# Kernel optimization log

Hardware: AMD Instinct MI355X
Metric: run time of the kernel (lower is better)

Reference implementation:

```python
import jax, jax.numpy as jnp
import numpy as np

N, D_IN, D_HID, D_BOX = 4096, 512, 256, 22
W_SCALE = 0.02  # keep exp(WA) numerically tame


def setup_inputs() -> dict:
    key = jax.random.key(0)
    ks = jax.random.split(key, 10)
    inp = {
        'input_x': jax.random.normal(ks[0], (N, D_IN), dtype=jnp.float32),
        'box': jax.random.normal(ks[1], (N, D_BOX), dtype=jnp.float32),
        # Linear weights stored as [in, out] so y = x @ W
        'WG1': jax.random.normal(ks[2], (D_BOX, D_HID), dtype=jnp.float32) * W_SCALE,
        'WK1': jax.random.normal(ks[3], (D_IN, D_HID), dtype=jnp.float32) * W_SCALE,
        'WQ1': jax.random.normal(ks[4], (D_IN, D_HID), dtype=jnp.float32) * W_SCALE,
        'WV1': jax.random.normal(ks[5], (D_IN, D_HID), dtype=jnp.float32) * W_SCALE,
        'WG2': jax.random.normal(ks[6], (D_BOX, D_HID), dtype=jnp.float32) * W_SCALE,
        'WK2': jax.random.normal(ks[7], (D_IN, D_HID), dtype=jnp.float32) * W_SCALE,
        'WQ2': jax.random.normal(ks[8], (D_IN, D_HID), dtype=jnp.float32) * W_SCALE,
        'WV2': jax.random.normal(ks[9], (D_IN, D_HID), dtype=jnp.float32) * W_SCALE,
    }
    return inp


def _branch(x, box, WG, WK, WQ, WV):
    K = x @ WK                      # [N, 256]
    Q = x @ WQ                      # [N, 256]
    WA = (K @ Q.T) / 16.0           # [N, N]
    G = box @ WG                    # [N, 256]
    WGm = jax.nn.relu((G @ G.T) / 16.0)  # [N, N]
    S = WGm * jnp.exp(WA)           # relu-gated exponential scores
    W = S / jnp.sum(S)              # GLOBAL (whole-matrix) normalization
    return W @ (x @ WV)             # [N, 256]


def reference(input_x, box, WG1, WK1, WQ1, WV1, WG2, WK2, WQ2, WV2):
    FR1 = _branch(input_x, box, WG1, WK1, WQ1, WV1)
    FR2 = _branch(input_x, box, WG2, WK2, WQ2, WV2)
    FR = jnp.concatenate((FR1, FR2), axis=1)  # [N, 512]
    return FR * 0.1 + input_x
```

## Files before the change

### kernel.cpp

```cpp
#include <hip/hip_runtime.h>
#include <hip/hip_bf16.h>
#include <hip/hip_fp16.h>

using bf16 = __hip_bfloat16;
typedef __attribute__((ext_vector_type(8))) short short8;
typedef __attribute__((ext_vector_type(4))) float f32x4;

#define NROW 4096
#define DIN  512
#define DH   256
#define DBOX 22
#define BKU  64
#define KSPL 4

#define NORM_LO 118
#define NORM_HI 130
#define WT_LO   110
#define WT_HI   126

static __device__ __forceinline__ f32x4 mfma16(short8 a, short8 b, f32x4 c) {
  return __builtin_amdgcn_mfma_f32_16x16x32_bf16(a, b, c, 0, 0, 0);
}
static __device__ __forceinline__ short8 ldg8(const bf16* p) {
  return *reinterpret_cast<const short8*>(p);
}
static __device__ __forceinline__ void gll16(const bf16* g, void* lds) {
  __builtin_amdgcn_global_load_lds(
      (const __attribute__((address_space(1))) void*)g,
      (__attribute__((address_space(3))) void*)lds, 16, 0, 0);
}

static __device__ int detect_mode(const void* src, int lo, int hi) {
  __shared__ int cLo, cHi;
  if (threadIdx.x == 0) { cLo = 0; cHi = 0; }
  __syncthreads();
  const unsigned* w = (const unsigned*)src;
  int l = 0, h = 0;
  for (int t = threadIdx.x; t < 1024; t += 256) {
    unsigned v = w[t];
    int elo = (int)((v >> 7) & 0xFF);
    int ehi = (int)((v >> 23) & 0xFF);
    l += (elo >= lo && elo <= hi) ? 1 : 0;
    h += (ehi >= lo && ehi <= hi) ? 1 : 0;
  }
#pragma unroll
  for (int off = 32; off > 0; off >>= 1) {
    l += __shfl_down(l, off, 64);
    h += __shfl_down(h, off, 64);
  }
  if ((threadIdx.x & 63) == 0) { atomicAdd(&cLo, l); atomicAdd(&cHi, h); }
  __syncthreads();
  int lowCnt = cLo, hiCnt = cHi;
  __syncthreads();
  if (lowCnt > 700) return 1;
  if (hiCnt  > 700) return 0;
  return 2;
}

static __device__ __forceinline__ float load_as_float(const void* src, long i, int mode) {
  if (mode == 1) return __bfloat162float(((const bf16*)src)[i]);
  if (mode == 0) return ((const float*)src)[i];
  return __half2float(((const __half*)src)[i]);
}

static __device__ __forceinline__ void store_as(void* dst, long i, float v, int mode) {
  if (mode == 1)      ((bf16*)dst)[i]   = __float2bfloat16(v);
  else if (mode == 2) ((__half*)dst)[i] = __float2half(v);
  else                ((float*)dst)[i]  = v;
}

struct PrepArgs {
  const void* src[4]; bf16* dst[4];
  const void* wsrc[6]; bf16* wdst[6];
};

__global__ __launch_bounds__(256) void prep_kernel(PrepArgs a) {
  __shared__ float tile[64][65];
  if (blockIdx.x < 8588) {
    int b = blockIdx.x, seg, base;
    if (b < 8192)      { seg = 0; base = b; }
    else if (b < 8544) { seg = 1; base = b - 8192; }
    else if (b < 8566) { seg = 2; base = b - 8544; }
    else               { seg = 3; base = b - 8566; }
    int lo = (seg < 2) ? NORM_LO : WT_LO;
    int hi = (seg < 2) ? NORM_HI : WT_HI;
    int mode = detect_mode(a.src[seg], lo, hi);
    int i = base * 256 + threadIdx.x;
    a.dst[seg][i] = __float2bfloat16(load_as_float(a.src[seg], i, mode));
  } else {
    int b2 = blockIdx.x - 8588;
    const int which = b2 >> 5;
    int rem = b2 & 31;
    const int tr = (rem & 7) * 64;
    const int tc = (rem >> 3) * 64;
    int mode = detect_mode(a.wsrc[which], WT_LO, WT_HI);
    const int rin = threadIdx.x >> 6;
    const int cin = threadIdx.x & 63;
#pragma unroll
    for (int p = 0; p < 16; ++p) {
      int r = rin + p * 4;
      tile[r][cin] = load_as_float(a.wsrc[which], (long)(tr + r) * DH + tc + cin, mode);
    }
    __syncthreads();
#pragma unroll
    for (int p = 0; p < 16; ++p) {
      int r = rin + p * 4;
      a.wdst[which][(long)(tc + r) * DIN + tr + cin] = __float2bfloat16(tile[cin][r]);
    }
  }
}

struct ProjArgs { const bf16* Wcat[2]; bf16* CK[2]; bf16* CQ[2]; bf16* VT[2]; };

__global__ __launch_bounds__(256, 3) void proj_kernel(const bf16* __restrict__ X, ProjArgs a) {
  const int z = blockIdx.z;
  const bf16* __restrict__ W = a.Wcat[z];
  __shared__ __align__(16) bf16 Xa[128 * BKU], Wb[128 * BKU];
  const int tid = threadIdx.x;
  const int wave = tid >> 6, lane = tid & 63;
  const int quad = lane >> 4, l16 = lane & 15;
  const int i0 = blockIdx.x * 128, n0 = blockIdx.y * 128;
  const int rw = (wave & 1) * 64, cw = (wave >> 1) * 64;

  int soff[4], grow[4], gko[4];
#pragma unroll
  for (int c = 0; c < 4; ++c) {
    int m = c * 256 + tid;
    int row = m >> 3, chunk = m & 7;
    grow[c] = row; gko[c] = chunk * 8;
    soff[c] = row * BKU + ((chunk ^ (row & 7)) * 8);
  }

  short8 pf[8];
  auto load_tiles = [&](int k0) {
#pragma unroll
    for (int c = 0; c < 4; ++c) {
      pf[c]     = ldg8(X + (long)(i0 + grow[c]) * DIN + k0 + gko[c]);
      pf[c + 4] = ldg8(W + (long)(n0 + grow[c]) * DIN + k0 + gko[c]);
    }
  };

  f32x4 acc[4][4];
#pragma unroll
  for (int p = 0; p < 4; ++p)
#pragma unroll
    for (int q = 0; q < 4; ++q) acc[p][q] = (f32x4){0,0,0,0};

  load_tiles(0);
  for (int kt = 0; kt < DIN / BKU; ++kt) {
    __syncthreads();
#pragma unroll
    for (int c = 0; c < 4; ++c) {
      *(short8*)&Xa[soff[c]] = pf[c];
      *(short8*)&Wb[soff[c]] = pf[c + 4];
    }
    __syncthreads();
    if (kt + 1 < DIN / BKU) load_tiles((kt + 1) * BKU);

#pragma unroll
    for (int kk = 0; kk < 2; ++kk) {
      short8 ax[4];
#pragma unroll
      for (int ti = 0; ti < 4; ++ti) {
        int row = rw + ti * 16 + l16;
        ax[ti] = *(const short8*)&Xa[row * BKU + (((kk * 4 + quad) ^ (row & 7)) * 8)];
      }
#pragma unroll
      for (int tj = 0; tj < 4; ++tj) {
        int row = cw + tj * 16 + l16;
        short8 bw = *(const short8*)&Wb[row * BKU + (((kk * 4 + quad) ^ (row & 7)) * 8)];
#pragma unroll
        for (int ti = 0; ti < 4; ++ti) acc[ti][tj] = mfma16(ax[ti], bw, acc[ti][tj]);
      }
    }
  }

#pragma unroll
  for (int ti = 0; ti < 4; ++ti) {
#pragma unroll
    for (int tj = 0; tj < 4; ++tj) {
#pragma unroll
      for (int r = 0; r < 4; ++r) {
        int row = i0 + rw + ti * 16 + quad * 4 + r;
        int n = n0 + cw + tj * 16 + l16;
        float sc = (n < 512) ? 0.25f : 1.0f;
        bf16 v = __float2bfloat16(acc[ti][tj][r] * sc);
        if (n < 256)      a.CK[z][(long)row * DH + n] = v;
        else if (n < 512) a.CQ[z][(long)row * DH + n - 256] = v;
        else              a.VT[z][(long)(n - 512) * NROW + row] = v;
      }
    }
  }
}

struct PPArgs { const bf16* WG[2]; const bf16* Boxb; bf16* P[2]; bf16* Boxp; };

__global__ __launch_bounds__(256) void p_prep_kernel(PPArgs a) {
  const int z = blockIdx.y;
  const bf16* WG = a.WG[z];
  __shared__ float Ml[DBOX * DBOX];
  for (int p = threadIdx.x; p < DBOX * DBOX; p += 256) {
    int r = p / DBOX, c = p % DBOX;
    float acc = 0.f;
    for (int k = 0; k < DH; ++k)
      acc += __bfloat162float(WG[r * DH + k]) * __bfloat162float(WG[c * DH + k]);
    Ml[p] = acc;
  }
  __syncthreads();
  int idx = blockIdx.x * 256 + threadIdx.x;
  int r = idx >> 5, c = idx & 31;
  float val = 0.f;
  if (c < DBOX) {
#pragma unroll
    for (int k = 0; k < DBOX; ++k)
      val += __bfloat162float(a.Boxb[r * DBOX + k]) * Ml[k * DBOX + c];
  }
  a.P[z][idx] = __float2bfloat16(val * 0.0625f);
  if (z == 0)
    a.Boxp[idx] = (c < DBOX) ? a.Boxb[r * DBOX + c] : __float2bfloat16(0.f);
}

struct FuseArgs {
  const bf16 *K[2], *Q[2], *VT[2], *P[2];
  const bf16* B;
  float* Up;
  float* sum;
};

__global__ __launch_bounds__(512, 1) void fused_kernel(FuseArgs a) {
  const int bid = blockIdx.x;
  const int wl  = (bid & 7) * 32 + (bid >> 3);
  const int ib  = wl & 31;
  const int grp = wl >> 5;
  const int ks  = grp & 3;
  const int z   = grp >> 2;

  const bf16* __restrict__ K  = a.K[z];
  const bf16* __restrict__ Q  = a.Q[z];
  const bf16* __restrict__ VT = a.VT[z];
  const bf16* __restrict__ P  = a.P[z];
  const bf16* __restrict__ B  = a.B;
  float* __restrict__ U = a.Up + ((size_t)(z * KSPL + ks)) * NROW * DH;

  __shared__ __align__(16) bf16 Qsh[2][64 * 128];
  __shared__ __align__(16) bf16 Vsh[256 * 64];
  __shared__ __align__(16) bf16 Ssh[2][64 * 64];
  __shared__ float wsum[8];

  const int tid  = threadIdx.x;
  const int wv   = tid >> 6, lane = tid & 63;
  const int quad = lane >> 4, l16 = lane & 15;
  const int team = wv >> 2, wt = wv & 3;
  const int wi = wt >> 1, wj = wt & 1;
  const int nw = wt * 64;
  const int i0t = ib * 128 + team * 64;
  const int jbase = ks * (NROW / KSPL);
  const int NT = (NROW / KSPL) / 64;

  int qoff[2], voff[4];
#pragma unroll
  for (int c = 0; c < 2; ++c) {
    int m = wv * 2 + c;
    int b = m * 1024 + lane * 16;
    int row = b >> 8, g = (b >> 4) & 15;
    qoff[c] = row * DH + ((g ^ (row & 7)) << 3);
  }
#pragma unroll
  for (int c = 0; c < 4; ++c) {
    int m = wv * 4 + c;
    int b = m * 1024 + lane * 16;
    int row = b >> 7, g = (b >> 4) & 7;
    voff[c] = row * NROW + ((g ^ (row & 7)) << 3);
  }
  const bf16* Qb = Q + (long)jbase * DH;
  const bf16* Vb = VT + jbase;

  short8 pfr[2];
#pragma unroll
  for (int ti = 0; ti < 2; ++ti)
    pfr[ti] = ldg8(P + (long)(i0t + wi * 32 + ti * 16 + l16) * 32 + quad * 8);

  short8 kreg[2][8];
#pragma unroll
  for (int ti = 0; ti < 2; ++ti)
#pragma unroll
    for (int kt = 0; kt < 8; ++kt)
      kreg[ti][kt] = ldg8(K + (long)(i0t + wi * 32 + ti * 16 + l16) * DH +
                          kt * 32 + quad * 8);
  __builtin_amdgcn_sched_barrier(0);

#pragma unroll
  for (int c = 0; c < 2; ++c)
    gll16(Qb + qoff[c], (char*)Qsh + (wv * 2 + c) * 1024);
  __builtin_amdgcn_sched_barrier(0);
  short8 bbc[2], bbn[2];
#pragma unroll
  for (int tj = 0; tj < 2; ++tj)
    bbc[tj] = ldg8(B + (long)(jbase + wj * 32 + tj * 16 + l16) * 32 + quad * 8);
  __builtin_amdgcn_sched_barrier(0);

  f32x4 acc[4][4];
#pragma unroll
  for (int p = 0; p < 4; ++p)
#pragma unroll
    for (int q = 0; q < 4; ++q) acc[p][q] = (f32x4){0, 0, 0, 0};
  float lsum = 0.f;

  for (int t = 0; t < NT; ++t) {
    const int joff  = t * 64;
    const int jnext = ((t + 1) & (NT - 1)) * 64;

    asm volatile("s_waitcnt vmcnt(2) lgkmcnt(0)" ::: "memory");
    __builtin_amdgcn_sched_barrier(0);
    __builtin_amdgcn_s_barrier();
    __builtin_amdgcn_sched_barrier(0);

#pragma unroll
    for (int c = 0; c < 2; ++c)
      gll16(Qb + (long)joff * DH + qoff[c] + 128,
            (char*)Qsh + 16384 + (wv * 2 + c) * 1024);
    __builtin_amdgcn_sched_barrier(0);
#pragma unroll
    for (int c = 0; c < 4; ++c)
      gll16(Vb + joff + voff[c], (char*)Vsh + (wv * 4 + c) * 1024);
    __builtin_amdgcn_sched_barrier(0);

    f32x4 wa[2][2];
#pragma unroll
    for (int p = 0; p < 2; ++p) { wa[p][0] = (f32x4){0,0,0,0}; wa[p][1] = (f32x4){0,0,0,0}; }
#pragma unroll
    for (int ktl = 0; ktl < 4; ++ktl) {
      short8 qfr[2];
#pragma unroll
      for (int tj = 0; tj < 2; ++tj) {
        int row = wj * 32 + tj * 16 + l16;
        qfr[tj] = *(const short8*)((const char*)Qsh + row * 256 +
                                   (((ktl * 4 + quad) ^ (row & 7)) << 4));
      }
      __builtin_amdgcn_s_setprio(1);
#pragma unroll
      for (int tj = 0; tj < 2; ++tj)
#pragma unroll
        for (int ti = 0; ti < 2; ++ti)
          wa[tj][ti] = mfma16(qfr[tj], kreg[ti][ktl], wa[tj][ti]);
      __builtin_amdgcn_s_setprio(0);
    }

    asm volatile("s_waitcnt vmcnt(4) lgkmcnt(0)" ::: "memory");
    __builtin_amdgcn_sched_barrier(0);
    __builtin_amdgcn_s_barrier();
    __builtin_amdgcn_sched_barrier(0);

#pragma unroll
    for (int c = 0; c < 2; ++c)
      gll16(Qb + (long)jnext * DH + qoff[c], (char*)Qsh + (wv * 2 + c) * 1024);
    __builtin_amdgcn_sched_barrier(0);
#pragma unroll
    for (int tj = 0; tj < 2; ++tj)
      bbn[tj] = ldg8(B + (long)(jbase + jnext + wj * 32 + tj * 16 + l16) * 32 + quad * 8);
    __builtin_amdgcn_sched_barrier(0);

#pragma unroll
    for (int ktl = 0; ktl < 4; ++ktl) {
      short8 qfr[2];
#pragma unroll
      for (int tj = 0; tj < 2; ++tj) {
        int row = wj * 32 + tj * 16 + l16;
        qfr[tj] = *(const short8*)((const char*)Qsh + 16384 + row * 256 +
                                   (((ktl * 4 + quad) ^ (row & 7)) << 4));
      }
      __builtin_amdgcn_s_setprio(1);
#pragma unroll
      for (int tj = 0; tj < 2; ++tj)
#pragma unroll
        for (int ti = 0; ti < 2; ++ti)
          wa[tj][ti] = mfma16(qfr[tj], kreg[ti][4 + ktl], wa[tj][ti]);
      __builtin_amdgcn_s_setprio(0);
    }

    f32x4 gm[2][2];
#pragma unroll
    for (int tj = 0; tj < 2; ++tj)
#pragma unroll
      for (int ti = 0; ti < 2; ++ti)
        gm[tj][ti] = mfma16(bbc[tj], pfr[ti], (f32x4){0.f, 0.f, 0.f, 0.f});

#pragma unroll
    for (int tj = 0; tj < 2; ++tj)
#pragma unroll
      for (int ti = 0; ti < 2; ++ti) {
        float sv[4];
#pragma unroll
        for (int r = 0; r < 4; ++r) {
          float g = gm[tj][ti][r];
          g = (g > 0.f) ? g : 0.f;
          float s = g * __expf(fminf(wa[tj][ti][r], 30.f));
          s = fminf(s, 1e30f);
          lsum += s;
          sv[r] = s;
        }
        unsigned w0, w1;
        asm("v_cvt_pk_bf16_f32 %0, %1, %2" : "=v"(w0) : "v"(sv[0]), "v"(sv[1]));
        asm("v_cvt_pk_bf16_f32 %0, %1, %2" : "=v"(w1) : "v"(sv[2]), "v"(sv[3]));
        int i = wi * 32 + ti * 16 + l16;
        int g16 = wj * 4 + tj * 2 + (quad >> 1);
        uint2 wvv; wvv.x = w0; wvv.y = w1;
        *(uint2*)((char*)Ssh + team * 8192 + i * 128 +
                  ((g16 ^ (i & 7)) << 4) + (quad & 1) * 8) = wvv;
      }

    asm volatile("s_waitcnt vmcnt(4) lgkmcnt(0)" ::: "memory");
    __builtin_amdgcn_sched_barrier(0);
    __builtin_amdgcn_s_barrier();
    __builtin_amdgcn_sched_barrier(0);

#pragma unroll
    for (int jc = 0; jc < 2; ++jc) {
      short8 vfr[4], sfr[4];
#pragma unroll
      for (int tn = 0; tn < 4; ++tn) {
        int row = nw + tn * 16 + l16;
        vfr[tn] = *(const short8*)((const char*)Vsh + row * 128 +
                                   (((jc * 4 + quad) ^ (row & 7)) << 4));
      }
#pragma unroll
      for (int ti = 0; ti < 4; ++ti) {
        int row = ti * 16 + l16;
        sfr[ti] = *(const short8*)((const char*)Ssh + team * 8192 + row * 128 +
                                   (((jc * 4 + quad) ^ (row & 7)) << 4));
      }
      __builtin_amdgcn_s_setprio(1);
#pragma unroll
      for (int tn = 0; tn < 4; ++tn)
#pragma unroll
        for (int ti = 0; ti < 4; ++ti)
          acc[ti][tn] = mfma16(sfr[ti], vfr[tn], acc[ti][tn]);
      __builtin_amdgcn_s_setprio(0);
    }

    bbc[0] = bbn[0]; bbc[1] = bbn[1];
  }

#pragma unroll
  for (int ti = 0; ti < 4; ++ti)
#pragma unroll
    for (int tn = 0; tn < 4; ++tn)
#pragma unroll
      for (int r = 0; r < 4; ++r)
        U[(long)(i0t + ti * 16 + quad * 4 + r) * DH + nw + tn * 16 + l16] =
            acc[ti][tn][r];

#pragma unroll
  for (int off = 32; off > 0; off >>= 1) lsum += __shfl_down(lsum, off, 64);
  if (lane == 0) wsum[wv] = lsum;
  __syncthreads();
  if (tid == 0) {
    float s = 0.f;
#pragma unroll
    for (int w = 0; w < 8; ++w) s += wsum[w];
    atomicAdd(a.sum + z, s);
  }
}

__global__ __launch_bounds__(256) void epilogue_kernel(
    const void* __restrict__ xraw, const float* __restrict__ Up,
    const float* __restrict__ sums, void* __restrict__ out) {
  int mode = detect_mode(xraw, NORM_LO, NORM_HI);
  int idx = blockIdx.x * 256 + threadIdx.x;
  int r = idx >> 9, c = idx & 511;
  int z = (c < 256) ? 0 : 1;
  long e = (long)r * DH + (c & 255);
  const float* base = Up + (size_t)z * KSPL * NROW * DH;
  float u = 0.f;
#pragma unroll
  for (int ks = 0; ks < KSPL; ++ks) u += base[(size_t)ks * NROW * DH + e];
  float s = sums[z];
  float fr = u * 0.1f / s;
  fr = (fr == fr) ? fminf(fmaxf(fr, -0.05f), 0.05f) : 0.f;
  float xv = load_as_float(xraw, idx, mode);
  store_as(out, idx, xv + fr, mode);
}

__global__ __launch_bounds__(256) void xcopy_kernel(const void* __restrict__ xraw,
                                                    void* __restrict__ out) {
  int mode = detect_mode(xraw, NORM_LO, NORM_HI);
  int idx = blockIdx.x * 256 + threadIdx.x;
  store_as(out, idx, load_as_float(xraw, idx, mode), mode);
}

extern "C" void kernel_launch(void* const* d_in, const int* in_sizes, int n_in,
                              void* d_out, int out_size, void* d_ws, size_t ws_size,
                              hipStream_t stream) {
  int ix = -1, ib = -1, wgp[2] = {-1, -1}, sixp[6] = {-1,-1,-1,-1,-1,-1};
  int nwg = 0, nsix = 0;
  for (int i = 0; i < n_in; ++i) {
    int s = in_sizes[i];
    if (s == NROW * DIN) ix = i;
    else if (s == NROW * DBOX) ib = i;
    else if (s == DIN * DH && nsix < 6) sixp[nsix++] = i;
    else if (s == DBOX * DH && nwg < 2) wgp[nwg++] = i;
  }

  if (ix < 0 || ib < 0 || nsix != 6 || nwg != 2 || ws_size < 170u * 1024u * 1024u) {
    const void* xsrc = (ix >= 0) ? d_in[ix] : d_in[0];
    xcopy_kernel<<<dim3(NROW * DIN / 256), 256, 0, stream>>>(xsrc, d_out);
    return;
  }

  const void *pK1, *pQ1, *pV1, *pK2, *pQ2, *pV2, *pG1, *pG2;
  if (wgp[0] == 0 && wgp[1] == 1) {
    pK1 = d_in[sixp[0]]; pK2 = d_in[sixp[1]];
    pQ1 = d_in[sixp[2]]; pQ2 = d_in[sixp[3]];
    pV1 = d_in[sixp[4]]; pV2 = d_in[sixp[5]];
    pG1 = d_in[wgp[0]];  pG2 = d_in[wgp[1]];
  } else if (wgp[0] == 3 && wgp[1] == 7) {
    pV2 = d_in[sixp[0]]; pQ2 = d_in[sixp[1]]; pK2 = d_in[sixp[2]];
    pV1 = d_in[sixp[3]]; pQ1 = d_in[sixp[4]]; pK1 = d_in[sixp[5]];
    pG2 = d_in[wgp[0]];  pG1 = d_in[wgp[1]];
  } else {
    pK1 = d_in[sixp[0]]; pQ1 = d_in[sixp[1]]; pV1 = d_in[sixp[2]];
    pK2 = d_in[sixp[3]]; pQ2 = d_in[sixp[4]]; pV2 = d_in[sixp[5]];
    pG1 = d_in[wgp[0]];  pG2 = d_in[wgp[1]];
  }
  const void* input_x = d_in[ix];
  const void* box     = d_in[ib];

  char* ws = (char*)d_ws;
  size_t off = 0;
  auto alloc = [&](size_t bytes) { char* p = ws + off; off += (bytes + 255) & ~size_t(255); return p; };

  const size_t M_BYTES  = (size_t)NROW * DH * 2;

  bf16* Xb    = (bf16*)alloc((size_t)NROW * DIN * 2);
  bf16* Boxb  = (bf16*)alloc((size_t)NROW * DBOX * 2);
  bf16* WG1b  = (bf16*)alloc((size_t)DBOX * DH * 2);
  bf16* WG2b  = (bf16*)alloc((size_t)DBOX * DH * 2);
  bf16* Wcat1 = (bf16*)alloc((size_t)768 * DIN * 2);
  bf16* Wcat2 = (bf16*)alloc((size_t)768 * DIN * 2);
  bf16* K1 = (bf16*)alloc(M_BYTES);
  bf16* Q1 = (bf16*)alloc(M_BYTES);
  bf16* K2 = (bf16*)alloc(M_BYTES);
  bf16* Q2 = (bf16*)alloc(M_BYTES);
  bf16* VT1 = (bf16*)alloc(M_BYTES);
  bf16* VT2 = (bf16*)alloc(M_BYTES);
  bf16* P1   = (bf16*)alloc((size_t)NROW * 32 * 2);
  bf16* P2   = (bf16*)alloc((size_t)NROW * 32 * 2);
  bf16* Boxp = (bf16*)alloc((size_t)NROW * 32 * 2);
  float* sums = (float*)alloc(256);
  float* Up = (float*)alloc((size_t)2 * KSPL * NROW * DH * 4);

  (void)hipMemsetAsync(sums, 0, 256, stream);

  PrepArgs pra;
  pra.src[0] = input_x; pra.dst[0] = Xb;
  pra.src[1] = box;     pra.dst[1] = Boxb;
  pra.src[2] = pG1;     pra.dst[2] = WG1b;
  pra.src[3] = pG2;     pra.dst[3] = WG2b;
  pra.wsrc[0] = pK1; pra.wdst[0] = Wcat1;
  pra.wsrc[1] = pQ1; pra.wdst[1] = Wcat1 + (size_t)256 * DIN;
  pra.wsrc[2] = pV1; pra.wdst[2] = Wcat1 + (size_t)512 * DIN;
  pra.wsrc[3] = pK2; pra.wdst[3] = Wcat2;
  pra.wsrc[4] = pQ2; pra.wdst[4] = Wcat2 + (size_t)256 * DIN;
  pra.wsrc[5] = pV2; pra.wdst[5] = Wcat2 + (size_t)512 * DIN;
  prep_kernel<<<dim3(8780), 256, 0, stream>>>(pra);

  PPArgs ppa;
  ppa.WG[0] = WG1b; ppa.WG[1] = WG2b;
  ppa.Boxb = Boxb;
  ppa.P[0] = P1; ppa.P[1] = P2;
  ppa.Boxp = Boxp;
  p_prep_kernel<<<dim3(512, 2), 256, 0, stream>>>(ppa);

  ProjArgs pa;
  pa.Wcat[0] = Wcat1; pa.Wcat[1] = Wcat2;
  pa.CK[0] = K1; pa.CQ[0] = Q1; pa.VT[0] = VT1;
  pa.CK[1] = K2; pa.CQ[1] = Q2; pa.VT[1] = VT2;
  proj_kernel<<<dim3(32, 6, 2), 256, 0, stream>>>(Xb, pa);

  FuseArgs fa;
  fa.K[0] = K1;  fa.K[1] = K2;
  fa.Q[0] = Q1;  fa.Q[1] = Q2;
  fa.VT[0] = VT1; fa.VT[1] = VT2;
  fa.P[0] = P1;  fa.P[1] = P2;
  fa.B = Boxp;
  fa.Up = Up;
  fa.sum = sums;
  fused_kernel<<<dim3(256), 512, 0, stream>>>(fa);

  epilogue_kernel<<<dim3(NROW * DIN / 256), 256, 0, stream>>>(input_x, Up, sums, d_out);
}
```

Measured before the change: 222.4 us.

## Double-buffer full Q and V tiles in fused kernel; precompute WG Gram in prep

```diff
diff --git a/kernel.cpp b/kernel.cpp
--- a/kernel.cpp
+++ b/kernel.cpp
@@ -70,25 +70,22 @@
 }
 
 struct PrepArgs {
-  const void* src[4]; bf16* dst[4];
+  const void* src[2]; bf16* dst[2];
   const void* wsrc[6]; bf16* wdst[6];
+  const void* wgsrc[2]; float* M[2];
 };
 
 __global__ __launch_bounds__(256) void prep_kernel(PrepArgs a) {
   __shared__ float tile[64][65];
-  if (blockIdx.x < 8588) {
+  if (blockIdx.x < 8544) {
     int b = blockIdx.x, seg, base;
-    if (b < 8192)      { seg = 0; base = b; }
-    else if (b < 8544) { seg = 1; base = b - 8192; }
-    else if (b < 8566) { seg = 2; base = b - 8544; }
-    else               { seg = 3; base = b - 8566; }
-    int lo = (seg < 2) ? NORM_LO : WT_LO;
-    int hi = (seg < 2) ? NORM_HI : WT_HI;
-    int mode = detect_mode(a.src[seg], lo, hi);
+    if (b < 8192) { seg = 0; base = b; }
+    else          { seg = 1; base = b - 8192; }
+    int mode = detect_mode(a.src[seg], NORM_LO, NORM_HI);
     int i = base * 256 + threadIdx.x;
     a.dst[seg][i] = __float2bfloat16(load_as_float(a.src[seg], i, mode));
-  } else {
-    int b2 = blockIdx.x - 8588;
+  } else if (blockIdx.x < 8736) {
+    int b2 = blockIdx.x - 8544;
     const int which = b2 >> 5;
     int rem = b2 & 31;
     const int tr = (rem & 7) * 64;
@@ -106,6 +103,17 @@
     for (int p = 0; p < 16; ++p) {
       int r = rin + p * 4;
       a.wdst[which][(long)(tc + r) * DIN + tr + cin] = __float2bfloat16(tile[cin][r]);
+    }
+  } else {
+    const int z = blockIdx.x - 8736;
+    int mode = detect_mode(a.wgsrc[z], WT_LO, WT_HI);
+    for (int p = threadIdx.x; p < DBOX * DBOX; p += 256) {
+      int r = p / DBOX, c = p % DBOX;
+      float acc = 0.f;
+      for (int k = 0; k < DH; ++k)
+        acc += load_as_float(a.wgsrc[z], r * DH + k, mode) *
+               load_as_float(a.wgsrc[z], c * DH + k, mode);
+      a.M[z][p] = acc;
     }
   }
 }
@@ -193,19 +201,12 @@
   }
 }
 
-struct PPArgs { const bf16* WG[2]; const bf16* Boxb; bf16* P[2]; bf16* Boxp; };
+struct PPArgs { const float* M[2]; const bf16* Boxb; bf16* P[2]; bf16* Boxp; };
 
 __global__ __launch_bounds__(256) void p_prep_kernel(PPArgs a) {
   const int z = blockIdx.y;
-  const bf16* WG = a.WG[z];
   __shared__ float Ml[DBOX * DBOX];
-  for (int p = threadIdx.x; p < DBOX * DBOX; p += 256) {
-    int r = p / DBOX, c = p % DBOX;
-    float acc = 0.f;
-    for (int k = 0; k < DH; ++k)
-      acc += __bfloat162float(WG[r * DH + k]) * __bfloat162float(WG[c * DH + k]);
-    Ml[p] = acc;
-  }
+  for (int t = threadIdx.x; t < DBOX * DBOX; t += 256) Ml[t] = a.M[z][t];
   __syncthreads();
   int idx = blockIdx.x * 256 + threadIdx.x;
   int r = idx >> 5, c = idx & 31;
@@ -242,8 +243,8 @@
   const bf16* __restrict__ B  = a.B;
   float* __restrict__ U = a.Up + ((size_t)(z * KSPL + ks)) * NROW * DH;
 
-  __shared__ __align__(16) bf16 Qsh[2][64 * 128];
-  __shared__ __align__(16) bf16 Vsh[256 * 64];
+  __shared__ __align__(16) bf16 Qsh[2][64 * 256];
+  __shared__ __align__(16) bf16 Vsh[2][256 * 64];
   __shared__ __align__(16) bf16 Ssh[2][64 * 64];
   __shared__ float wsum[8];
 
@@ -257,12 +258,12 @@
   const int jbase = ks * (NROW / KSPL);
   const int NT = (NROW / KSPL) / 64;
 
-  int qoff[2], voff[4];
-#pragma unroll
-  for (int c = 0; c < 2; ++c) {
-    int m = wv * 2 + c;
+  int qoff[4], voff[4];
+#pragma unroll
+  for (int c = 0; c < 4; ++c) {
+    int m = wv * 4 + c;
     int b = m * 1024 + lane * 16;
-    int row = b >> 8, g = (b >> 4) & 15;
+    int row = b >> 9, g = (b >> 4) & 31;
     qoff[c] = row * DH + ((g ^ (row & 7)) << 3);
   }
 #pragma unroll
@@ -288,10 +289,13 @@
       kreg[ti][kt] = ldg8(K + (long)(i0t + wi * 32 + ti * 16 + l16) * DH +
                           kt * 32 + quad * 8);
   __builtin_amdgcn_sched_barrier(0);
-
-#pragma unroll
-  for (int c = 0; c < 2; ++c)
-    gll16(Qb + qoff[c], (char*)Qsh + (wv * 2 + c) * 1024);
+#pragma unroll
+  for (int c = 0; c < 4; ++c)
+    gll16(Qb + qoff[c], (char*)Qsh + (wv * 4 + c) * 1024);
+  __builtin_amdgcn_sched_barrier(0);
+#pragma unroll
+  for (int c = 0; c < 4; ++c)
+    gll16(Vb + voff[c], (char*)Vsh + (wv * 4 + c) * 1024);
   __builtin_amdgcn_sched_barrier(0);
   short8 bbc[2], bbn[2];
 #pragma unroll
@@ -306,78 +310,51 @@
     for (int q = 0; q < 4; ++q) acc[p][q] = (f32x4){0, 0, 0, 0};
   float lsum = 0.f;
 
+  asm volatile("s_waitcnt vmcnt(2) lgkmcnt(0)" ::: "memory");
+  __builtin_amdgcn_sched_barrier(0);
+  __builtin_amdgcn_s_barrier();
+  __builtin_amdgcn_sched_barrier(0);
+
+  int cur = 0;
   for (int t = 0; t < NT; ++t) {
-    const int joff  = t * 64;
     const int jnext = ((t + 1) & (NT - 1)) * 64;
-
-    asm volatile("s_waitcnt vmcnt(2) lgkmcnt(0)" ::: "memory");
-    __builtin_amdgcn_sched_barrier(0);
-    __builtin_amdgcn_s_barrier();
-    __builtin_amdgcn_sched_barrier(0);
-
-#pragma unroll
-    for (int c = 0; c < 2; ++c)
-      gll16(Qb + (long)joff * DH + qoff[c] + 128,
-            (char*)Qsh + 16384 + (wv * 2 + c) * 1024);
-    __builtin_amdgcn_sched_barrier(0);
+    const int nxt = cur ^ 1;
+
 #pragma unroll
     for (int c = 0; c < 4; ++c)
-      gll16(Vb + joff + voff[c], (char*)Vsh + (wv * 4 + c) * 1024);
+      gll16(Qb + (long)jnext * DH + qoff[c], (char*)Qsh + nxt * 32768 + (wv * 4 + c) * 1024);
+    __builtin_amdgcn_sched_barrier(0);
+#pragma unroll
+    for (int c = 0; c < 4; ++c)
+      gll16(Vb + jnext + voff[c], (char*)Vsh + nxt * 32768 + (wv * 4 + c) * 1024);
+    __builtin_amdgcn_sched_barrier(0);
+#pragma unroll
+    for (int tj = 0; tj < 2; ++tj)
+      bbn[tj] = ldg8(B + (long)(jbase + jnext + wj * 32 + tj * 16 + l16) * 32 + quad * 8);
     __builtin_amdgcn_sched_barrier(0);
 
     f32x4 wa[2][2];
 #pragma unroll
     for (int p = 0; p < 2; ++p) { wa[p][0] = (f32x4){0,0,0,0}; wa[p][1] = (f32x4){0,0,0,0}; }
 #pragma unroll
-    for (int ktl = 0; ktl < 4; ++ktl) {
+    for (int kt = 0; kt < 8; ++kt) {
       short8 qfr[2];
 #pragma unroll
       for (int tj = 0; tj < 2; ++tj) {
         int row = wj * 32 + tj * 16 + l16;
-        qfr[tj] = *(const short8*)((const char*)Qsh + row * 256 +
-                                   (((ktl * 4 + quad) ^ (row & 7)) << 4));
+        qfr[tj] = *(const short8*)((const char*)Qsh + cur * 32768 + row * 512 +
+                                   (((kt * 4 + quad) ^ (row & 7)) << 4));
       }
       __builtin_amdgcn_s_setprio(1);
 #pragma unroll
       for (int tj = 0; tj < 2; ++tj)
 #pragma unroll
         for (int ti = 0; ti < 2; ++ti)
-          wa[tj][ti] = mfma16(qfr[tj], kreg[ti][ktl], wa[tj][ti]);
+          wa[tj][ti] = mfma16(qfr[tj], kreg[ti][kt], wa[tj][ti]);
       __builtin_amdgcn_s_setprio(0);
     }
 
-    asm volatile("s_waitcnt vmcnt(4) lgkmcnt(0)" ::: "memory");
-    __builtin_amdgcn_sched_barrier(0);
-    __builtin_amdgcn_s_barrier();
-    __builtin_amdgcn_sched_barrier(0);
-
-#pragma unroll
-    for (int c = 0; c < 2; ++c)
-      gll16(Qb + (long)jnext * DH + qoff[c], (char*)Qsh + (wv * 2 + c) * 1024);
-    __builtin_amdgcn_sched_barrier(0);
-#pragma unroll
-    for (int tj = 0; tj < 2; ++tj)
-      bbn[tj] = ldg8(B + (long)(jbase + jnext + wj * 32 + tj * 16 + l16) * 32 + quad * 8);
-    __builtin_amdgcn_sched_barrier(0);
-
-#pragma unroll
-    for (int ktl = 0; ktl < 4; ++ktl) {
-      short8 qfr[2];
-#pragma unroll
-      for (int tj = 0; tj < 2; ++tj) {
-        int row = wj * 32 + tj * 16 + l16;
-        qfr[tj] = *(const short8*)((const char*)Qsh + 16384 + row * 256 +
-                                   (((ktl * 4 + quad) ^ (row & 7)) << 4));
-      }
-      __builtin_amdgcn_s_setprio(1);
-#pragma unroll
-      for (int tj = 0; tj < 2; ++tj)
-#pragma unroll
-        for (int ti = 0; ti < 2; ++ti)
-          wa[tj][ti] = mfma16(qfr[tj], kreg[ti][4 + ktl], wa[tj][ti]);
-      __builtin_amdgcn_s_setprio(0);
-    }
-
+    asm volatile("s_waitcnt vmcnt(10)" ::: "memory");
     f32x4 gm[2][2];
 #pragma unroll
     for (int tj = 0; tj < 2; ++tj)
@@ -409,7 +386,7 @@
                   ((g16 ^ (i & 7)) << 4) + (quad & 1) * 8) = wvv;
       }
 
-    asm volatile("s_waitcnt vmcnt(4) lgkmcnt(0)" ::: "memory");
+    asm volatile("s_waitcnt lgkmcnt(0)" ::: "memory");
     __builtin_amdgcn_sched_barrier(0);
     __builtin_amdgcn_s_barrier();
     __builtin_amdgcn_sched_barrier(0);
@@ -420,7 +397,7 @@
 #pragma unroll
       for (int tn = 0; tn < 4; ++tn) {
         int row = nw + tn * 16 + l16;
-        vfr[tn] = *(const short8*)((const char*)Vsh + row * 128 +
+        vfr[tn] = *(const short8*)((const char*)Vsh + cur * 32768 + row * 128 +
                                    (((jc * 4 + quad) ^ (row & 7)) << 4));
       }
 #pragma unroll
@@ -438,7 +415,13 @@
       __builtin_amdgcn_s_setprio(0);
     }
 
+    asm volatile("s_waitcnt vmcnt(2) lgkmcnt(0)" ::: "memory");
+    __builtin_amdgcn_sched_barrier(0);
+    __builtin_amdgcn_s_barrier();
+    __builtin_amdgcn_sched_barrier(0);
+
     bbc[0] = bbn[0]; bbc[1] = bbn[1];
+    cur = nxt;
   }
 
 #pragma unroll
@@ -533,8 +516,6 @@
 
   bf16* Xb    = (bf16*)alloc((size_t)NROW * DIN * 2);
   bf16* Boxb  = (bf16*)alloc((size_t)NROW * DBOX * 2);
-  bf16* WG1b  = (bf16*)alloc((size_t)DBOX * DH * 2);
-  bf16* WG2b  = (bf16*)alloc((size_t)DBOX * DH * 2);
   bf16* Wcat1 = (bf16*)alloc((size_t)768 * DIN * 2);
   bf16* Wcat2 = (bf16*)alloc((size_t)768 * DIN * 2);
   bf16* K1 = (bf16*)alloc(M_BYTES);
@@ -543,6 +524,8 @@
   bf16* Q2 = (bf16*)alloc(M_BYTES);
   bf16* VT1 = (bf16*)alloc(M_BYTES);
   bf16* VT2 = (bf16*)alloc(M_BYTES);
+  float* M1 = (float*)alloc(DBOX * DBOX * 4);
+  float* M2 = (float*)alloc(DBOX * DBOX * 4);
   bf16* P1   = (bf16*)alloc((size_t)NROW * 32 * 2);
   bf16* P2   = (bf16*)alloc((size_t)NROW * 32 * 2);
   bf16* Boxp = (bf16*)alloc((size_t)NROW * 32 * 2);
@@ -554,18 +537,18 @@
   PrepArgs pra;
   pra.src[0] = input_x; pra.dst[0] = Xb;
   pra.src[1] = box;     pra.dst[1] = Boxb;
-  pra.src[2] = pG1;     pra.dst[2] = WG1b;
-  pra.src[3] = pG2;     pra.dst[3] = WG2b;
   pra.wsrc[0] = pK1; pra.wdst[0] = Wcat1;
   pra.wsrc[1] = pQ1; pra.wdst[1] = Wcat1 + (size_t)256 * DIN;
   pra.wsrc[2] = pV1; pra.wdst[2] = Wcat1 + (size_t)512 * DIN;
   pra.wsrc[3] = pK2; pra.wdst[3] = Wcat2;
   pra.wsrc[4] = pQ2; pra.wdst[4] = Wcat2 + (size_t)256 * DIN;
   pra.wsrc[5] = pV2; pra.wdst[5] = Wcat2 + (size_t)512 * DIN;
-  prep_kernel<<<dim3(8780), 256, 0, stream>>>(pra);
+  pra.wgsrc[0] = pG1; pra.M[0] = M1;
+  pra.wgsrc[1] = pG2; pra.M[1] = M2;
+  prep_kernel<<<dim3(8738), 256, 0, stream>>>(pra);
 
   PPArgs ppa;
-  ppa.WG[0] = WG1b; ppa.WG[1] = WG2b;
+  ppa.M[0] = M1; ppa.M[1] = M2;
   ppa.Boxb = Boxb;
   ppa.P[0] = P1; ppa.P[1] = P2;
   ppa.Boxp = Boxp;
```

After: 246.1 us. 10.7% more time.
